# Kernel tuning notes

Hardware: AMD Instinct MI355X
Metric: run time of the kernel (lower is better)

The kernel has to match this reference:

```python
import jax, jax.numpy as jnp
import numpy as np

N_HEADS = 16
EPS = 1e-6

def _feature_map(x):
    return jax.nn.elu(x) + 1.0

def setup_inputs() -> dict:
    key = jax.random.key(0)
    k1, k2, k3 = jax.random.split(key, 3)
    B, S, D = 1, 2048, 1024
    x = jax.random.normal(k1, (B, S, D), dtype=jnp.float32)
    causal_mask = jnp.tril(jnp.ones((S, S), dtype=bool))[None, None]  # (1,1,S,S)
    # scale weights like nn.Linear default init (roughly 1/sqrt(fan_in))
    W_qkv = jax.random.normal(k2, (D, 3 * D), dtype=jnp.float32) / np.sqrt(D)
    W_out = jax.random.normal(k3, (D, D), dtype=jnp.float32) / np.sqrt(D)
    return {"x": x, "causal_mask": causal_mask, "W_qkv": W_qkv, "W_out": W_out}

def reference(x, causal_mask, W_qkv, W_out):
    B, S, D = x.shape
    H = N_HEADS
    hd = D // H
    qkv = x @ W_qkv                              # (B,S,3D)
    q, k, v = jnp.split(qkv, 3, axis=-1)
    def to_heads(t):
        return t.reshape(B, S, H, hd).transpose(0, 2, 1, 3)  # (B,H,S,hd)
    q, k, v = to_heads(q), to_heads(k), to_heads(v)
    phi_q = _feature_map(q)
    phi_k = _feature_map(k)
    k_cum = jnp.cumsum(phi_k, axis=2)                        # (B,H,S,hd)
    kv = jnp.einsum('bhsi,bhsj->bhsij', phi_k, v)            # (B,H,S,hd,hd)
    kv_cum = jnp.cumsum(kv, axis=2)
    numer = jnp.einsum('bhsi,bhsij->bhsj', phi_q, kv_cum)    # (B,H,S,hd)
    denom = jnp.einsum('bhsi,bhsi->bhs', phi_q, k_cum) + EPS
    attn_out = numer / denom[..., None]
    attn_out = attn_out.transpose(0, 2, 1, 3).reshape(B, S, D)
    return attn_out @ W_out
```

## Files before the change

### kernel.cpp

```cpp
#include <hip/hip_runtime.h>
#include <cstddef>
#include <cstdint>

#define SEQ 2048
#define DIM 1024
#define NH 16
#define HD 64
#define CK 64
#define NCK (SEQ / CK)
#define KVR 65
#define KVRP 80

typedef __attribute__((ext_vector_type(8))) short short8;
typedef __attribute__((ext_vector_type(8))) unsigned short ushort8;
typedef __attribute__((ext_vector_type(4))) float fx4;

__device__ __forceinline__ float phi_fn(float x) {
    return x > 0.f ? x + 1.f : __expf(x);
}
__device__ __forceinline__ float bf2f(unsigned short u) {
    return __uint_as_float((unsigned int)u << 16);
}
__device__ __forceinline__ unsigned short f2bf(float f) {
    unsigned int u = __float_as_uint(f);
    unsigned int r = (u + 0x7FFFu + ((u >> 16) & 1u)) >> 16;
    return (unsigned short)r;
}

__device__ __forceinline__ void lds_write16(unsigned short* base, int row, int col, short8 v) {
    int byte = row * 128 + col * 2; byte ^= (row & 7) << 4;
    *(short8*)((char*)base + byte) = v;
}
__device__ __forceinline__ void lds_write2(unsigned short* base, int row, int col, unsigned short v) {
    int byte = row * 128 + col * 2; byte ^= (row & 7) << 4;
    *(unsigned short*)((char*)base + byte) = v;
}
__device__ __forceinline__ short8 lds_read_frag(const unsigned short* base, int row, int kcol) {
    int byte = row * 128 + kcol * 2; byte ^= (row & 7) << 4;
    return *(const short8*)((const char*)base + byte);
}

template<int N> __device__ __forceinline__ void waitv() {
    if constexpr (N == 0)       asm volatile("s_waitcnt vmcnt(0)"  ::: "memory");
    else if constexpr (N == 4)  asm volatile("s_waitcnt vmcnt(4)"  ::: "memory");
    else if constexpr (N == 5)  asm volatile("s_waitcnt vmcnt(5)"  ::: "memory");
    else if constexpr (N == 6)  asm volatile("s_waitcnt vmcnt(6)"  ::: "memory");
    else if constexpr (N == 8)  asm volatile("s_waitcnt vmcnt(8)"  ::: "memory");
    else if constexpr (N == 10) asm volatile("s_waitcnt vmcnt(10)" ::: "memory");
    else if constexpr (N == 12) asm volatile("s_waitcnt vmcnt(12)" ::: "memory");
    else                        asm volatile("s_waitcnt vmcnt(0)"  ::: "memory");
}

__global__ __launch_bounds__(256)
void prep_fused(const float* __restrict__ x, unsigned short* __restrict__ xb,
                const float* __restrict__ W1, unsigned short* __restrict__ WT1,
                const float* __restrict__ W2, unsigned short* __restrict__ WT2)
{
    __shared__ float t[32][33];
    int b = blockIdx.x;
    if (b < 2048) {
        const int i = (b * 256 + threadIdx.x) * 4;
        float4 v = *(const float4*)&x[i];
        ushort4 o;
        o.x = f2bf(v.x); o.y = f2bf(v.y); o.z = f2bf(v.z); o.w = f2bf(v.w);
        *(ushort4*)&xb[i] = o;
        return;
    }
    b -= 2048;
    const float* W; unsigned short* WT; int N, kb, nb;
    if (b < 96 * 32) {
        W = W1; WT = WT1; N = 3 * DIM;
        nb = (b % 96) * 32; kb = (b / 96) * 32;
    } else {
        b -= 96 * 32;
        W = W2; WT = WT2; N = DIM;
        nb = (b % 32) * 32; kb = (b / 32) * 32;
    }
    const int c = threadIdx.x & 31, r0 = threadIdx.x >> 5;
    #pragma unroll
    for (int i = 0; i < 4; ++i) {
        const int r = r0 + i * 8;
        t[r][c] = W[(size_t)(kb + r) * N + nb + c];
    }
    __syncthreads();
    #pragma unroll
    for (int i = 0; i < 4; ++i) {
        const int r = r0 + i * 8;
        WT[(size_t)(nb + r) * DIM + kb + c] = f2bf(t[c][r]);
    }
}

template<int WAVES_M, int WAVES_N, int NFRAG, int OUT_BF16>
__global__ __launch_bounds__(WAVES_M * WAVES_N * 64)
void gemm_pipe(const unsigned short* __restrict__ A,
               const unsigned short* __restrict__ BT,
               void* __restrict__ Cout, int M, int N, int K)
{
    constexpr int BN      = WAVES_N * NFRAG * 16;
    constexpr int THREADS = WAVES_M * WAVES_N * 64;
    constexpr int CHUNK   = THREADS * 16;
    constexpr int ALOADS  = (128 * 64 * 2) / CHUNK;
    constexpr int BLOADS  = (BN * 64 * 2) / CHUNK;
    constexpr int LOADS   = ALOADS + BLOADS;

    __shared__ unsigned short As[3][128 * 64];
    __shared__ unsigned short Bs[3][BN * 64];

    const int tid = threadIdx.x, lane = tid & 63, wave = tid >> 6;
    const int wm = (wave / WAVES_N) * 64;
    const int wn = (wave % WAVES_N) * (NFRAG * 16);

    int wg = blockIdx.y * gridDim.x + blockIdx.x;
    const int cpx = (gridDim.x * gridDim.y) >> 3;
    wg = (wg & 7) * cpx + (wg >> 3);
    const int bx = wg / gridDim.y;
    const int by = wg % gridDim.y;

    const int m0 = by * 128, n0 = bx * BN;
    const unsigned short* Abase = A + (size_t)m0 * K;
    const unsigned short* Bbase = BT + (size_t)n0 * K;
    const int nt = K >> 6;
    const int fr = lane & 15, fk = (lane >> 4) * 8;

    fx4 acc[4][NFRAG] = {};

    auto STAGE = [&](int slot, int t) {
        const int k0 = t << 6;
        #pragma unroll
        for (int q = 0; q < ALOADS; ++q) {
            const int L = q * CHUNK + tid * 16;
            const int row = L >> 7;
            const int srcb = L ^ ((row & 7) << 4);
            const unsigned short* g = Abase + (size_t)row * K + k0 + ((srcb & 127) >> 1);
            __builtin_amdgcn_global_load_lds(
                (const __attribute__((address_space(1))) void*)g,
                (__attribute__((address_space(3))) void*)((char*)&As[slot][0] + q * CHUNK + wave * 1024),
                16, 0, 0);
        }
        #pragma unroll
        for (int q = 0; q < BLOADS; ++q) {
            const int L = q * CHUNK + tid * 16;
            const int row = L >> 7;
            const int srcb = L ^ ((row & 7) << 4);
            const unsigned short* g = Bbase + (size_t)row * K + k0 + ((srcb & 127) >> 1);
            __builtin_amdgcn_global_load_lds(
                (const __attribute__((address_space(1))) void*)g,
                (__attribute__((address_space(3))) void*)((char*)&Bs[slot][0] + q * CHUNK + wave * 1024),
                16, 0, 0);
        }
    };

    STAGE(0, 0); STAGE(1, 1);
    waitv<LOADS>();
    __builtin_amdgcn_s_barrier();

    for (int t = 0; t < nt; ++t) {
        const int cur = t % 3;
        short8 a0[4], a1[4], b0[NFRAG], b1[NFRAG];
        #pragma unroll
        for (int i = 0; i < 4; ++i) {
            a0[i] = lds_read_frag(&As[cur][0], wm + i * 16 + fr, fk);
            a1[i] = lds_read_frag(&As[cur][0], wm + i * 16 + fr, 32 + fk);
        }
        #pragma unroll
        for (int j = 0; j < NFRAG; ++j) {
            b0[j] = lds_read_frag(&Bs[cur][0], wn + j * 16 + fr, fk);
            b1[j] = lds_read_frag(&Bs[cur][0], wn + j * 16 + fr, 32 + fk);
        }

        const bool pf = (t + 2 < nt);
        if (pf) STAGE((t + 2) % 3, t + 2);

        asm volatile("s_waitcnt lgkmcnt(0)" ::: "memory");
        __builtin_amdgcn_sched_barrier(0);

        __builtin_amdgcn_s_setprio(1);
        #pragma unroll
        for (int i = 0; i < 4; ++i)
            #pragma unroll
            for (int j = 0; j < NFRAG; ++j)
                acc[i][j] = __builtin_amdgcn_mfma_f32_16x16x32_bf16(a0[i], b0[j], acc[i][j], 0, 0, 0);
        #pragma unroll
        for (int i = 0; i < 4; ++i)
            #pragma unroll
            for (int j = 0; j < NFRAG; ++j)
                acc[i][j] = __builtin_amdgcn_mfma_f32_16x16x32_bf16(a1[i], b1[j], acc[i][j], 0, 0, 0);
        __builtin_amdgcn_s_setprio(0);

        if (pf) waitv<LOADS>(); else waitv<0>();
        __builtin_amdgcn_s_barrier();
    }

    const int cr = (lane >> 4) * 4, cc = lane & 15;
    #pragma unroll
    for (int i = 0; i < 4; ++i)
        #pragma unroll
        for (int j = 0; j < NFRAG; ++j) {
            const int m = m0 + wm + i * 16 + cr;
            const int n = n0 + wn + j * 16 + cc;
            #pragma unroll
            for (int r = 0; r < 4; ++r) {
                const float v = acc[i][j][r];
                if (OUT_BF16)
                    ((unsigned short*)Cout)[(size_t)(m + r) * N + n] = f2bf(v);
                else
                    ((float*)Cout)[(size_t)(m + r) * N + n] = v;
            }
        }
}

__global__ __launch_bounds__(256)
void chunk_kv(const unsigned short* __restrict__ qkv, float* __restrict__ kvs)
{
    const int c = blockIdx.x, h = blockIdx.y;
    __shared__ unsigned short kT[64 * 64];
    __shared__ unsigned short vT[KVRP * 64];
    const int tid = threadIdx.x, lane = tid & 63, wave = tid >> 6;
    const int s0 = c * CK;

    #pragma unroll
    for (int part = 0; part < 2; ++part) {
        const int s = (tid >> 3) + part * 32;
        const int d0 = (tid & 7) * 8;
        const size_t base = (size_t)(s0 + s) * (3 * DIM) + (size_t)h * HD + d0;
        ushort8 kk = *(const ushort8*)&qkv[base + DIM];
        ushort8 vv = *(const ushort8*)&qkv[base + 2 * DIM];
        #pragma unroll
        for (int u = 0; u < 8; ++u) {
            lds_write2(kT, d0 + u, s, f2bf(phi_fn(bf2f(kk[u]))));
            lds_write2(vT, d0 + u, s, vv[u]);
        }
    }
    if (tid < 64) lds_write2(vT, 64, tid, 0x3F80);
    for (int idx = tid; idx < 15 * 64; idx += 256)
        lds_write2(vT, 65 + (idx >> 6), idx & 63, 0);
    __syncthreads();

    fx4 acc[5] = {};
    #pragma unroll
    for (int ks = 0; ks < 2; ++ks) {
        short8 b = lds_read_frag(kT, wave * 16 + (lane & 15), ks * 32 + (lane >> 4) * 8);
        #pragma unroll
        for (int mt = 0; mt < 5; ++mt) {
            short8 a = lds_read_frag(vT, mt * 16 + (lane & 15), ks * 32 + (lane >> 4) * 8);
            acc[mt] = __builtin_amdgcn_mfma_f32_16x16x32_bf16(a, b, acc[mt], 0, 0, 0);
        }
    }
    float* dst = kvs + (size_t)(h * NCK + c) * KVR * 64;
    const int i = wave * 16 + (lane & 15);
    #pragma unroll
    for (int mt = 0; mt < 5; ++mt)
        #pragma unroll
        for (int t = 0; t < 4; ++t) {
            const int j = mt * 16 + (lane >> 4) * 4 + t;
            if (j < KVR) dst[(size_t)j * 64 + i] = acc[mt][t];
        }
}

__global__ __launch_bounds__(256)
void scan_kv(const float* __restrict__ kvs, unsigned short* __restrict__ kvpb)
{
    const int e = blockIdx.x * 256 + threadIdx.x;
    if (e >= NH * KVR * 64) return;
    const int h = e / (KVR * 64), off = e % (KVR * 64);
    const float* src = kvs + (size_t)h * NCK * KVR * 64 + off;
    unsigned short* dst = kvpb + (size_t)h * NCK * KVR * 64 + off;
    float v[NCK];
    #pragma unroll
    for (int c2 = 0; c2 < NCK; ++c2) v[c2] = src[(size_t)c2 * KVR * 64];
    float run = 0.f;
    #pragma unroll
    for (int c2 = 0; c2 < NCK; ++c2) {
        dst[(size_t)c2 * KVR * 64] = f2bf(run);
        run += v[c2];
    }
}

__global__ __launch_bounds__(256)
void attn_chunk(const unsigned short* __restrict__ qkv,
                const unsigned short* __restrict__ kvpb,
                unsigned short* __restrict__ attnb)
{
    const int c = blockIdx.x, h = blockIdx.y;
    __shared__ unsigned short q_s[64 * 64];
    __shared__ unsigned short k_s[64 * 64];
    __shared__ unsigned short p_s[64 * 64];
    __shared__ unsigned short vT[KVRP * 64];
    __shared__ unsigned short kvp[KVRP * 64];
    const int tid = threadIdx.x, lane = tid & 63, wave = tid >> 6;
    const int s0 = c * CK;

    #pragma unroll
    for (int part = 0; part < 2; ++part) {
        const int s = (tid >> 3) + part * 32;
        const int d0 = (tid & 7) * 8;
        const size_t base = (size_t)(s0 + s) * (3 * DIM) + (size_t)h * HD + d0;
        ushort8 qq = *(const ushort8*)&qkv[base];
        ushort8 kk = *(const ushort8*)&qkv[base + DIM];
        ushort8 vv = *(const ushort8*)&qkv[base + 2 * DIM];
        short8 qo, ko;
        #pragma unroll
        for (int u = 0; u < 8; ++u) {
            qo[u] = (short)f2bf(phi_fn(bf2f(qq[u])));
            ko[u] = (short)f2bf(phi_fn(bf2f(kk[u])));
        }
        lds_write16(q_s, s, d0, qo);
        lds_write16(k_s, s, d0, ko);
        #pragma unroll
        for (int u = 0; u < 8; ++u)
            lds_write2(vT, d0 + u, s, vv[u]);
    }
    const unsigned short* kv_src = kvpb + (size_t)(h * NCK + c) * KVR * 64;
    for (int idx = tid * 8; idx < KVR * 64; idx += 2048) {
        ushort8 kv8 = *(const ushort8*)&kv_src[idx];
        short8 kv8s;
        #pragma unroll
        for (int u = 0; u < 8; ++u) kv8s[u] = (short)kv8[u];
        lds_write16(kvp, idx >> 6, idx & 63, kv8s);
    }
    if (tid < 64) lds_write2(vT, 64, tid, 0x3F80);
    for (int idx = tid; idx < 15 * 64; idx += 256) {
        lds_write2(vT, 65 + (idx >> 6), idx & 63, 0);
        lds_write2(kvp, 65 + (idx >> 6), idx & 63, 0);
    }
    __syncthreads();

    const int r0 = wave * 16;
    fx4 accp[4] = {};
    #pragma unroll
    for (int ks = 0; ks < 2; ++ks) {
        short8 aq = lds_read_frag(q_s, r0 + (lane & 15), ks * 32 + (lane >> 4) * 8);
        #pragma unroll
        for (int nt = 0; nt < 4; ++nt) {
            short8 bk = lds_read_frag(k_s, nt * 16 + (lane & 15), ks * 32 + (lane >> 4) * 8);
            accp[nt] = __builtin_amdgcn_mfma_f32_16x16x32_bf16(aq, bk, accp[nt], 0, 0, 0);
        }
    }
    #pragma unroll
    for (int nt = 0; nt < 4; ++nt)
        #pragma unroll
        for (int t = 0; t < 4; ++t) {
            const int r = r0 + (lane >> 4) * 4 + t, sc = nt * 16 + (lane & 15);
            lds_write2(p_s, r, sc, (sc <= r) ? f2bf(accp[nt][t]) : (unsigned short)0);
        }
    __syncthreads();

    fx4 acc[5] = {};
    #pragma unroll
    for (int ks = 0; ks < 2; ++ks) {
        short8 ap = lds_read_frag(p_s, r0 + (lane & 15), ks * 32 + (lane >> 4) * 8);
        short8 aq = lds_read_frag(q_s, r0 + (lane & 15), ks * 32 + (lane >> 4) * 8);
        #pragma unroll
        for (int nt = 0; nt < 5; ++nt) {
            short8 bv  = lds_read_frag(vT,  nt * 16 + (lane & 15), ks * 32 + (lane >> 4) * 8);
            short8 bkv = lds_read_frag(kvp, nt * 16 + (lane & 15), ks * 32 + (lane >> 4) * 8);
            acc[nt] = __builtin_amdgcn_mfma_f32_16x16x32_bf16(ap, bv,  acc[nt], 0, 0, 0);
            acc[nt] = __builtin_amdgcn_mfma_f32_16x16x32_bf16(aq, bkv, acc[nt], 0, 0, 0);
        }
    }
    float dinv[4];
    #pragma unroll
    for (int t = 0; t < 4; ++t) {
        const float d = __shfl(acc[4][t], lane & 48, 64);
        dinv[t] = 1.f / (d + 1e-6f);
    }
    #pragma unroll
    for (int nt = 0; nt < 4; ++nt)
        #pragma unroll
        for (int t = 0; t < 4; ++t) {
            const int r = r0 + (lane >> 4) * 4 + t, j = nt * 16 + (lane & 15);
            attnb[(size_t)(s0 + r) * DIM + (size_t)h * HD + j] = f2bf(acc[nt][t] * dinv[t]);
        }
}

extern "C" void kernel_launch(void* const* d_in, const int* in_sizes, int n_in,
                              void* d_out, int out_size, void* d_ws, size_t ws_size,
                              hipStream_t stream)
{
    const float* x     = (const float*)d_in[0];
    const float* W_qkv = (const float*)d_in[2];
    const float* W_out = (const float*)d_in[3];
    float* out = (float*)d_out;

    char* ws = (char*)d_ws;
    size_t off = 0;
    unsigned short* qkvb = (unsigned short*)(ws + off); off += (size_t)SEQ * 3 * DIM * 2;
    unsigned short* xb   = (unsigned short*)(ws + off); off += (size_t)SEQ * DIM * 2;
    float*          kvs  = (float*)         (ws + off); off += (size_t)NH * NCK * KVR * 64 * 4;
    unsigned short* kvpb = (unsigned short*)(ws + off); off += (size_t)NH * NCK * KVR * 64 * 2;
    unsigned short* wqt  = (unsigned short*)(ws + off); off += (size_t)3 * DIM * DIM * 2;
    unsigned short* wot  = (unsigned short*)(ws + off); off += (size_t)DIM * DIM * 2;
    unsigned short* attnb = xb;

    dim3 blk(256);

    prep_fused<<<dim3(2048 + 96 * 32 + 32 * 32), blk, 0, stream>>>(
        x, xb, W_qkv, wqt, W_out, wot);

    gemm_pipe<2, 4, 3, 1><<<dim3(3 * DIM / 192, SEQ / 128), dim3(512), 0, stream>>>(
        xb, wqt, qkvb, SEQ, 3 * DIM, DIM);

    chunk_kv<<<dim3(NCK, NH), blk, 0, stream>>>(qkvb, kvs);
    scan_kv<<<dim3((NH * KVR * 64 + 255) / 256), blk, 0, stream>>>(kvs, kvpb);
    attn_chunk<<<dim3(NCK, NH), blk, 0, stream>>>(qkvb, kvpb, attnb);

    gemm_pipe<2, 2, 2, 0><<<dim3(DIM / 64, SEQ / 128), dim3(256), 0, stream>>>(
        attnb, wot, out, SEQ, DIM, DIM);
}
```

Measured before the change: 58.74 us.

## Fuse chunk KV, scan and attention into one cooperative kernel; 4-slot QKV GEMM pipeline

Merges the three attention-stage kernels into one cooperative launch with grid-wide syncs between chunk-KV, prefix scan and chunk attention. Staged K^T and V^T stay in LDS across the syncs, so the attention phase no longer reloads V. Separately, the QKV GEMM moves to a 4-slot LDS ring with a deeper prefetch distance. The cooperative launch requires all 512 blocks to be co-resident. The larger GEMM LDS footprint may reduce occupancy.

Measured after the change: 170.4 us. +190.0%, slower.

```diff
diff --git a/kernel.cpp b/kernel.cpp
--- a/kernel.cpp
+++ b/kernel.cpp
@@ -1,6 +1,9 @@
 #include <hip/hip_runtime.h>
+#include <hip/hip_cooperative_groups.h>
 #include <cstddef>
 #include <cstdint>
+
+namespace cg = cooperative_groups;
 
 #define SEQ 2048
 #define DIM 1024
@@ -90,7 +93,7 @@
     }
 }
 
-template<int WAVES_M, int WAVES_N, int NFRAG, int OUT_BF16>
+template<int WAVES_M, int WAVES_N, int NFRAG, int SLOTS, int OUT_BF16>
 __global__ __launch_bounds__(WAVES_M * WAVES_N * 64)
 void gemm_pipe(const unsigned short* __restrict__ A,
                const unsigned short* __restrict__ BT,
@@ -103,8 +106,8 @@
     constexpr int BLOADS  = (BN * 64 * 2) / CHUNK;
     constexpr int LOADS   = ALOADS + BLOADS;
 
-    __shared__ unsigned short As[3][128 * 64];
-    __shared__ unsigned short Bs[3][BN * 64];
+    __shared__ unsigned short As[SLOTS][128 * 64];
+    __shared__ unsigned short Bs[SLOTS][BN * 64];
 
     const int tid = threadIdx.x, lane = tid & 63, wave = tid >> 6;
     const int wm = (wave / WAVES_N) * 64;
@@ -151,11 +154,12 @@
     };
 
     STAGE(0, 0); STAGE(1, 1);
-    waitv<LOADS>();
+    if constexpr (SLOTS == 4) STAGE(2, 2);
+    waitv<(SLOTS - 2) * LOADS>();
     __builtin_amdgcn_s_barrier();
 
     for (int t = 0; t < nt; ++t) {
-        const int cur = t % 3;
+        const int cur = (SLOTS == 4) ? (t & 3) : (t % 3);
         short8 a0[4], a1[4], b0[NFRAG], b1[NFRAG];
         #pragma unroll
         for (int i = 0; i < 4; ++i) {
@@ -168,8 +172,11 @@
             b1[j] = lds_read_frag(&Bs[cur][0], wn + j * 16 + fr, 32 + fk);
         }
 
-        const bool pf = (t + 2 < nt);
-        if (pf) STAGE((t + 2) % 3, t + 2);
+        const bool pf = (t + SLOTS - 1 < nt);
+        if (pf) {
+            const int ns = (SLOTS == 4) ? ((t + 3) & 3) : ((t + 2) % 3);
+            STAGE(ns, t + SLOTS - 1);
+        }
 
         asm volatile("s_waitcnt lgkmcnt(0)" ::: "memory");
         __builtin_amdgcn_sched_barrier(0);
@@ -187,7 +194,14 @@
                 acc[i][j] = __builtin_amdgcn_mfma_f32_16x16x32_bf16(a1[i], b1[j], acc[i][j], 0, 0, 0);
         __builtin_amdgcn_s_setprio(0);
 
-        if (pf) waitv<LOADS>(); else waitv<0>();
+        if constexpr (SLOTS == 4) {
+            if (t + 3 < nt)      waitv<2 * LOADS>();
+            else if (t + 2 < nt) waitv<LOADS>();
+            else                 waitv<0>();
+        } else {
+            if (t + 2 < nt)      waitv<LOADS>();
+            else                 waitv<0>();
+        }
         __builtin_amdgcn_s_barrier();
     }
 
@@ -210,14 +224,23 @@
 }
 
 __global__ __launch_bounds__(256)
-void chunk_kv(const unsigned short* __restrict__ qkv, float* __restrict__ kvs)
+void attn_fused(const unsigned short* __restrict__ qkv, float* __restrict__ kvs,
+                unsigned short* __restrict__ kvpb, unsigned short* __restrict__ attnb)
 {
-    const int c = blockIdx.x, h = blockIdx.y;
-    __shared__ unsigned short kT[64 * 64];
-    __shared__ unsigned short vT[KVRP * 64];
+    cg::grid_group grid = cg::this_grid();
+    __shared__ unsigned short pool[22528];
+    unsigned short* q_s = pool;
+    unsigned short* k_s = pool + 4096;
+    unsigned short* p_s = pool + 8192;
+    unsigned short* vT  = pool + 12288;
+    unsigned short* kvp = pool + 17408;
+
+    const int blk = blockIdx.x;
+    const int c = blk & 31, h = blk >> 5;
     const int tid = threadIdx.x, lane = tid & 63, wave = tid >> 6;
     const int s0 = c * CK;
 
+    unsigned short* kT = q_s;
     #pragma unroll
     for (int part = 0; part < 2; ++part) {
         const int s = (tid >> 3) + part * 32;
@@ -236,59 +259,47 @@
         lds_write2(vT, 65 + (idx >> 6), idx & 63, 0);
     __syncthreads();
 
-    fx4 acc[5] = {};
-    #pragma unroll
-    for (int ks = 0; ks < 2; ++ks) {
-        short8 b = lds_read_frag(kT, wave * 16 + (lane & 15), ks * 32 + (lane >> 4) * 8);
-        #pragma unroll
-        for (int mt = 0; mt < 5; ++mt) {
-            short8 a = lds_read_frag(vT, mt * 16 + (lane & 15), ks * 32 + (lane >> 4) * 8);
-            acc[mt] = __builtin_amdgcn_mfma_f32_16x16x32_bf16(a, b, acc[mt], 0, 0, 0);
-        }
-    }
-    float* dst = kvs + (size_t)(h * NCK + c) * KVR * 64;
-    const int i = wave * 16 + (lane & 15);
-    #pragma unroll
-    for (int mt = 0; mt < 5; ++mt)
-        #pragma unroll
-        for (int t = 0; t < 4; ++t) {
-            const int j = mt * 16 + (lane >> 4) * 4 + t;
-            if (j < KVR) dst[(size_t)j * 64 + i] = acc[mt][t];
-        }
-}
-
-__global__ __launch_bounds__(256)
-void scan_kv(const float* __restrict__ kvs, unsigned short* __restrict__ kvpb)
-{
-    const int e = blockIdx.x * 256 + threadIdx.x;
-    if (e >= NH * KVR * 64) return;
-    const int h = e / (KVR * 64), off = e % (KVR * 64);
-    const float* src = kvs + (size_t)h * NCK * KVR * 64 + off;
-    unsigned short* dst = kvpb + (size_t)h * NCK * KVR * 64 + off;
-    float v[NCK];
-    #pragma unroll
-    for (int c2 = 0; c2 < NCK; ++c2) v[c2] = src[(size_t)c2 * KVR * 64];
-    float run = 0.f;
-    #pragma unroll
-    for (int c2 = 0; c2 < NCK; ++c2) {
-        dst[(size_t)c2 * KVR * 64] = f2bf(run);
-        run += v[c2];
-    }
-}
-
-__global__ __launch_bounds__(256)
-void attn_chunk(const unsigned short* __restrict__ qkv,
-                const unsigned short* __restrict__ kvpb,
-                unsigned short* __restrict__ attnb)
-{
-    const int c = blockIdx.x, h = blockIdx.y;
-    __shared__ unsigned short q_s[64 * 64];
-    __shared__ unsigned short k_s[64 * 64];
-    __shared__ unsigned short p_s[64 * 64];
-    __shared__ unsigned short vT[KVRP * 64];
-    __shared__ unsigned short kvp[KVRP * 64];
-    const int tid = threadIdx.x, lane = tid & 63, wave = tid >> 6;
-    const int s0 = c * CK;
+    {
+        fx4 acc[5] = {};
+        #pragma unroll
+        for (int ks = 0; ks < 2; ++ks) {
+            short8 b = lds_read_frag(kT, wave * 16 + (lane & 15), ks * 32 + (lane >> 4) * 8);
+            #pragma unroll
+            for (int mt = 0; mt < 5; ++mt) {
+                short8 a = lds_read_frag(vT, mt * 16 + (lane & 15), ks * 32 + (lane >> 4) * 8);
+                acc[mt] = __builtin_amdgcn_mfma_f32_16x16x32_bf16(a, b, acc[mt], 0, 0, 0);
+            }
+        }
+        float* dst = kvs + (size_t)(h * NCK + c) * KVR * 64;
+        const int i = wave * 16 + (lane & 15);
+        #pragma unroll
+        for (int mt = 0; mt < 5; ++mt)
+            #pragma unroll
+            for (int t = 0; t < 4; ++t) {
+                const int j = mt * 16 + (lane >> 4) * 4 + t;
+                if (j < KVR) dst[(size_t)j * 64 + i] = acc[mt][t];
+            }
+    }
+    grid.sync();
+
+    {
+        const int e = blk * 256 + tid;
+        if (e < NH * KVR * 64) {
+            const int hh = e / (KVR * 64), off = e % (KVR * 64);
+            const float* src = kvs + (size_t)hh * NCK * KVR * 64 + off;
+            unsigned short* dst = kvpb + (size_t)hh * NCK * KVR * 64 + off;
+            float v[NCK];
+            #pragma unroll
+            for (int c2 = 0; c2 < NCK; ++c2) v[c2] = src[(size_t)c2 * KVR * 64];
+            float run = 0.f;
+            #pragma unroll
+            for (int c2 = 0; c2 < NCK; ++c2) {
+                dst[(size_t)c2 * KVR * 64] = f2bf(run);
+                run += v[c2];
+            }
+        }
+    }
+    grid.sync();
 
     #pragma unroll
     for (int part = 0; part < 2; ++part) {
@@ -297,7 +308,6 @@
         const size_t base = (size_t)(s0 + s) * (3 * DIM) + (size_t)h * HD + d0;
         ushort8 qq = *(const ushort8*)&qkv[base];
         ushort8 kk = *(const ushort8*)&qkv[base + DIM];
-        ushort8 vv = *(const ushort8*)&qkv[base + 2 * DIM];
         short8 qo, ko;
         #pragma unroll
         for (int u = 0; u < 8; ++u) {
@@ -306,22 +316,18 @@
         }
         lds_write16(q_s, s, d0, qo);
         lds_write16(k_s, s, d0, ko);
-        #pragma unroll
-        for (int u = 0; u < 8; ++u)
-            lds_write2(vT, d0 + u, s, vv[u]);
-    }
-    const unsigned short* kv_src = kvpb + (size_t)(h * NCK + c) * KVR * 64;
-    for (int idx = tid * 8; idx < KVR * 64; idx += 2048) {
-        ushort8 kv8 = *(const ushort8*)&kv_src[idx];
-        short8 kv8s;
-        #pragma unroll
-        for (int u = 0; u < 8; ++u) kv8s[u] = (short)kv8[u];
-        lds_write16(kvp, idx >> 6, idx & 63, kv8s);
-    }
-    if (tid < 64) lds_write2(vT, 64, tid, 0x3F80);
-    for (int idx = tid; idx < 15 * 64; idx += 256) {
-        lds_write2(vT, 65 + (idx >> 6), idx & 63, 0);
-        lds_write2(kvp, 65 + (idx >> 6), idx & 63, 0);
+    }
+    {
+        const unsigned short* kv_src = kvpb + (size_t)(h * NCK + c) * KVR * 64;
+        for (int idx = tid * 8; idx < KVR * 64; idx += 2048) {
+            ushort8 kv8 = *(const ushort8*)&kv_src[idx];
+            short8 kv8s;
+            #pragma unroll
+            for (int u = 0; u < 8; ++u) kv8s[u] = (short)kv8[u];
+            lds_write16(kvp, idx >> 6, idx & 63, kv8s);
+        }
+        for (int idx = tid; idx < 15 * 64; idx += 256)
+            lds_write2(kvp, 65 + (idx >> 6), idx & 63, 0);
     }
     __syncthreads();
 
@@ -397,13 +403,15 @@
     prep_fused<<<dim3(2048 + 96 * 32 + 32 * 32), blk, 0, stream>>>(
         x, xb, W_qkv, wqt, W_out, wot);
 
-    gemm_pipe<2, 4, 3, 1><<<dim3(3 * DIM / 192, SEQ / 128), dim3(512), 0, stream>>>(
+    gemm_pipe<2, 4, 3, 4, 1><<<dim3(3 * DIM / 192, SEQ / 128), dim3(512), 0, stream>>>(
         xb, wqt, qkvb, SEQ, 3 * DIM, DIM);
 
-    chunk_kv<<<dim3(NCK, NH), blk, 0, stream>>>(qkvb, kvs);
-    scan_kv<<<dim3((NH * KVR * 64 + 255) / 256), blk, 0, stream>>>(kvs, kvpb);
-    attn_chunk<<<dim3(NCK, NH), blk, 0, stream>>>(qkvb, kvpb, attnb);
-
-    gemm_pipe<2, 2, 2, 0><<<dim3(DIM / 64, SEQ / 128), dim3(256), 0, stream>>>(
+    {
+        void* args[] = {(void*)&qkvb, (void*)&kvs, (void*)&kvpb, (void*)&attnb};
+        hipLaunchCooperativeKernel((const void*)attn_fused, dim3(NCK * NH), dim3(256),
+                                   args, 0, stream);
+    }
+
+    gemm_pipe<2, 2, 2, 3, 0><<<dim3(DIM / 64, SEQ / 128), dim3(256), 0, stream>>>(
         attnb, wot, out, SEQ, DIM, DIM);
 }
```
